# Kernel optimization log

Measured on AMD Instinct MI355X. Metric: run time of the kernel, lower is better.

## Reference

```python
import jax, jax.numpy as jnp
import numpy as np

H = 512
V = 50000
S = 400
B = 64


def setup_inputs() -> dict:
    key = jax.random.key(0)
    ks = jax.random.split(key, 20)
    inp = {
        'input': jax.random.normal(ks[0], (1, B, H), jnp.float32),
        'encoder_states': jax.random.normal(ks[1], (S, B, H), jnp.float32),
        'oov_enc_mask': jax.random.randint(ks[2], (S, B), 0, 2, jnp.int32),
        'hidden': jnp.zeros((1, B, H), jnp.float32),
        # GRU params (PyTorch layout: gates ordered r, z, n)
        'W_ih': jax.random.normal(ks[3], (3 * H, H), jnp.float32) * 0.02,
        'W_hh': jax.random.normal(ks[4], (3 * H, H), jnp.float32) * 0.02,
        'b_ih': jax.random.normal(ks[5], (3 * H,), jnp.float32) * 0.02,
        'b_hh': jax.random.normal(ks[6], (3 * H,), jnp.float32) * 0.02,
        # output vocab projection Linear(2H, V)
        'out_W': jax.random.normal(ks[7], (V, 2 * H), jnp.float32) * 0.02,
        'out_b': jax.random.normal(ks[8], (V,), jnp.float32) * 0.02,
        # additive attention params
        'v': jax.random.normal(ks[9], (H, 1), jnp.float32) * 0.02,
        'Wh': jax.random.normal(ks[10], (H, H), jnp.float32) * 0.02,
        'Ws': jax.random.normal(ks[11], (H, H), jnp.float32) * 0.02,
        'b_attn': jax.random.normal(ks[12], (1, H), jnp.float32) * 0.02,
        # pointer probability Linears (H -> 1)
        'pWh': jax.random.normal(ks[13], (1, H), jnp.float32) * 0.02,
        'pWs': jax.random.normal(ks[14], (1, H), jnp.float32) * 0.02,
        'pWx': jax.random.normal(ks[15], (1, H), jnp.float32) * 0.02,
        'pWx_b': jax.random.normal(ks[16], (1,), jnp.float32) * 0.02,
    }
    return inp


def reference(input, encoder_states, oov_enc_mask, hidden,
              W_ih, W_hh, b_ih, b_hh, out_W, out_b,
              v, Wh, Ws, b_attn, pWh, pWs, pWx, pWx_b):
    x = input[0]            # (B, H)
    h0 = hidden[0]          # (B, H)

    # --- single-step GRU (PyTorch gate order r, z, n) ---
    gi = x @ W_ih.T + b_ih      # (B, 3H)
    gh = h0 @ W_hh.T + b_hh     # (B, 3H)
    ir, iz, inn = jnp.split(gi, 3, axis=1)
    hr, hz, hn = jnp.split(gh, 3, axis=1)
    r = jax.nn.sigmoid(ir + hr)
    z = jax.nn.sigmoid(iz + hz)
    n = jnp.tanh(inn + r * hn)
    h = (1.0 - z) * n + z * h0          # decoder_state, (B, H)
    hidden_new = h[None]                # (1, B, H)

    # --- Bahdanau additive attention, softmax over seq axis ---
    x1 = jnp.einsum('sbh,hk->sbk', encoder_states, Wh)   # (S, B, H)
    x2 = h @ Ws                                          # (B, H) broadcasts over S
    scores = jnp.squeeze(jnp.tanh(x1 + x2 + b_attn) @ v, 2)  # (S, B)
    attn = jax.nn.softmax(scores, axis=0)                # (S, B)
    attn_bs = attn.T                                     # (B, S)

    context = jnp.einsum('bs,sbh->bh', attn_bs, encoder_states)  # (B, H)
    global_state = jnp.concatenate([h, context], axis=1)         # (B, 2H)

    # --- pointer probability ---
    p = jax.nn.sigmoid(context @ pWh.T + h @ pWs.T + x @ pWx.T + pWx_b)  # (B, 1)

    vocab_distr = p * jax.nn.selu(global_state @ out_W.T + out_b)        # (B, V)
    oov_vocab_distr = (1.0 - p) * (attn_bs * oov_enc_mask.astype(jnp.float32).T)  # (B, S)
    extended_vocab_distr = jnp.concatenate([vocab_distr, oov_vocab_distr], axis=1)

    return extended_vocab_distr, hidden_new, jnp.squeeze(p), attn
```

## Files before the change

kernel.cpp:

```cpp
#include <hip/hip_runtime.h>
#include <cmath>

#define H    512
#define H2   1024
#define V    50000
#define SEQ  400
#define EXT  (V + SEQ)

typedef __attribute__((ext_vector_type(8))) short short8;
typedef __attribute__((ext_vector_type(4))) float floatx4;

__device__ __forceinline__ unsigned int bfpack2(float lo, float hi) {
    unsigned int a = __float_as_uint(lo) + 0x8000u;
    unsigned int b = __float_as_uint(hi) + 0x8000u;
    return __builtin_amdgcn_perm(b, a, 0x07060302);
}
__device__ __forceinline__ uint4 pack8(float4 a, float4 b) {
    uint4 r;
    r.x = bfpack2(a.x, a.y);
    r.y = bfpack2(a.z, a.w);
    r.z = bfpack2(b.x, b.y);
    r.w = bfpack2(b.z, b.w);
    return r;
}
__device__ __forceinline__ float4 ld4(const float* p) { return *(const float4*)p; }

__global__ __launch_bounds__(256) void k0_transpose(
    const float* __restrict__ Wh, const float* __restrict__ Ws,
    unsigned short* __restrict__ WhT, unsigned short* __restrict__ WsT)
{
    __shared__ float T[64][65];
    const float* src = blockIdx.z ? Ws : Wh;
    unsigned short* dst = blockIdx.z ? WsT : WhT;
    const int k0 = blockIdx.x * 64, n0 = blockIdx.y * 64;
    const int tid = threadIdx.x;
    #pragma unroll
    for (int i = 0; i < 16; ++i) {
        int e = i * 256 + tid;
        int r = e >> 6, c = e & 63;
        T[r][c] = src[(size_t)(k0 + r) * H + n0 + c];
    }
    __syncthreads();
    #pragma unroll
    for (int i = 0; i < 16; ++i) {
        int e = i * 256 + tid;
        int nn = e >> 6, kk = e & 63;
        unsigned int u = __float_as_uint(T[kk][nn]) + 0x8000u;
        dst[(size_t)(n0 + nn) * H + k0 + kk] = (unsigned short)(u >> 16);
    }
}

__global__ __launch_bounds__(256) void k1_gru_part(
    const float* __restrict__ x, const float* __restrict__ h0,
    const float* __restrict__ W_ih, const float* __restrict__ W_hh,
    float* __restrict__ gacc)
{
    __shared__ uint4 Ax[512];
    __shared__ uint4 Ah[512];
    __shared__ uint4 Bg[6][512];
    const int tid  = threadIdx.x;
    const int wave = tid >> 6, lane = tid & 63;
    const int lrow = lane & 15, q = lane >> 4;
    const int J0   = blockIdx.x * 64;
    const int ks   = blockIdx.y;
    const int kc   = ks * 64;

    #pragma unroll
    for (int c = 0; c < 2; ++c) {
        int idx = c * 256 + tid;
        int m = idx >> 3, j2 = idx & 7, k8 = j2 ^ (m & 7);
        const float* sx = x  + m * H + kc + k8 * 8;
        const float* sh = h0 + m * H + kc + k8 * 8;
        Ax[idx] = pack8(ld4(sx), ld4(sx + 4));
        Ah[idx] = pack8(ld4(sh), ld4(sh + 4));
    }
    #pragma unroll
    for (int g = 0; g < 6; ++g) {
        const float* Wb = (g < 3) ? W_ih : W_hh;
        const int go = (g % 3) * H;
        #pragma unroll
        for (int c = 0; c < 2; ++c) {
            int idx = c * 256 + tid;
            int n = idx >> 3, j2 = idx & 7, k8 = j2 ^ (n & 7);
            const float* sw = Wb + (size_t)(go + J0 + n) * H + kc + k8 * 8;
            Bg[g][idx] = pack8(ld4(sw), ld4(sw + 4));
        }
    }
    __syncthreads();

    floatx4 acc[6];
    #pragma unroll
    for (int g = 0; g < 6; ++g) acc[g] = (floatx4){0.f, 0.f, 0.f, 0.f};
    floatx4 accm[6][4];
    #pragma unroll
    for (int g = 0; g < 6; ++g)
        #pragma unroll
        for (int mt = 0; mt < 4; ++mt) accm[g][mt] = (floatx4){0.f, 0.f, 0.f, 0.f};

    #pragma unroll
    for (int kk8 = 0; kk8 < 8; kk8 += 4) {
        const int k8 = kk8 + q;
        short8 ax[4], ah[4];
        #pragma unroll
        for (int mt = 0; mt < 4; ++mt) {
            int m = mt * 16 + lrow;
            ax[mt] = *(const short8*)&Ax[m * 8 + (k8 ^ (m & 7))];
            ah[mt] = *(const short8*)&Ah[m * 8 + (k8 ^ (m & 7))];
        }
        const int n = wave * 16 + lrow;
        const int gidx = n * 8 + (k8 ^ (n & 7));
        #pragma unroll
        for (int g = 0; g < 6; ++g) {
            short8 bb = *(const short8*)&Bg[g][gidx];
            #pragma unroll
            for (int mt = 0; mt < 4; ++mt)
                accm[g][mt] = __builtin_amdgcn_mfma_f32_16x16x32_bf16(
                    (g < 3) ? ax[mt] : ah[mt], bb, accm[g][mt], 0, 0, 0);
        }
    }
    const int j = J0 + wave * 16 + lrow;
    #pragma unroll
    for (int g = 0; g < 6; ++g)
        #pragma unroll
        for (int mt = 0; mt < 4; ++mt)
            #pragma unroll
            for (int r = 0; r < 4; ++r) {
                const int bb = mt * 16 + q * 4 + r;
                gacc[(((size_t)g * 8 + ks) * 64 + bb) * H + j] = accm[g][mt][r];
            }
}

__global__ __launch_bounds__(256) void k1_gru_fin(
    const float* __restrict__ gacc, const float* __restrict__ h0,
    const float* __restrict__ b_ih, const float* __restrict__ b_hh,
    float* __restrict__ h_out)
{
    const int e = blockIdx.x * 256 + threadIdx.x;
    const int j = e & (H - 1);
    const int b = e >> 9;
    float gs[6];
    #pragma unroll
    for (int g = 0; g < 6; ++g) {
        float sum = 0.f;
        #pragma unroll
        for (int ks = 0; ks < 8; ++ks)
            sum += gacc[(((size_t)g * 8 + ks) * 64 + b) * H + j];
        gs[g] = sum;
    }
    float rg = 1.f / (1.f + expf(-(gs[0] + b_ih[j] + gs[3] + b_hh[j])));
    float zg = 1.f / (1.f + expf(-(gs[1] + b_ih[H + j] + gs[4] + b_hh[H + j])));
    float ng = tanhf(gs[2] + b_ih[2 * H + j] + rg * (gs[5] + b_hh[2 * H + j]));
    float h0v = h0[b * H + j];
    h_out[b * H + j] = (1.f - zg) * ng + zg * h0v;
}

__global__ __launch_bounds__(256) void k2_x2(
    const float* __restrict__ h, const unsigned short* __restrict__ WsT,
    const float* __restrict__ b_attn, float* __restrict__ x2)
{
    __shared__ uint4 Ag[512];
    __shared__ uint4 Bgg[512];
    const int tid  = threadIdx.x;
    const int wave = tid >> 6, lane = tid & 63;
    const int lrow = lane & 15, q = lane >> 4;
    const int n0   = blockIdx.x * 64;

    floatx4 acc[4];
    #pragma unroll
    for (int mt = 0; mt < 4; ++mt) acc[mt] = (floatx4){0.f, 0.f, 0.f, 0.f};

    for (int kc = 0; kc < H; kc += 64) {
        __syncthreads();
        #pragma unroll
        for (int c = 0; c < 2; ++c) {
            int idx = c * 256 + tid;
            int m = idx >> 3, j2 = idx & 7, k8 = j2 ^ (m & 7);
            const float* sh = h + m * H + kc + k8 * 8;
            Ag[idx] = pack8(ld4(sh), ld4(sh + 4));
            Bgg[idx] = *(const uint4*)(WsT + (size_t)(n0 + m) * H + kc + k8 * 8);
        }
        __syncthreads();
        #pragma unroll
        for (int kk8 = 0; kk8 < 8; kk8 += 4) {
            const int k8 = kk8 + q;
            const int n = wave * 16 + lrow;
            short8 bb = *(const short8*)&Bgg[n * 8 + (k8 ^ (n & 7))];
            #pragma unroll
            for (int mt = 0; mt < 4; ++mt) {
                int m = mt * 16 + lrow;
                short8 a = *(const short8*)&Ag[m * 8 + (k8 ^ (m & 7))];
                acc[mt] = __builtin_amdgcn_mfma_f32_16x16x32_bf16(a, bb, acc[mt], 0, 0, 0);
            }
        }
    }
    const int n = n0 + wave * 16 + lrow;
    const float ba = b_attn[n];
    #pragma unroll
    for (int mt = 0; mt < 4; ++mt)
        #pragma unroll
        for (int r = 0; r < 4; ++r) {
            const int bb = mt * 16 + q * 4 + r;
            x2[bb * H + n] = acc[mt][r] + ba;
        }
}

__global__ __launch_bounds__(256) void k3_scores(
    const float* __restrict__ enc, const unsigned short* __restrict__ WhT,
    const float* __restrict__ x2, const float* __restrict__ v,
    float* __restrict__ part)
{
    __shared__ uint4 AsG[512];
    __shared__ uint4 BsG[1024];
    __shared__ float red[256];
    const int s   = blockIdx.x;
    const int nc  = blockIdx.y;
    const int n0  = nc * 128;
    const int tid  = threadIdx.x;
    const int wave = tid >> 6, lane = tid & 63;
    const int lrow = lane & 15, q = lane >> 4;

    floatx4 acc[4][2];
    #pragma unroll
    for (int mt = 0; mt < 4; ++mt)
        #pragma unroll
        for (int nt = 0; nt < 2; ++nt) acc[mt][nt] = (floatx4){0.f, 0.f, 0.f, 0.f};

    const float* Abase = enc + (size_t)s * 64 * H;
    for (int kc = 0; kc < H; kc += 64) {
        __syncthreads();
        #pragma unroll
        for (int c = 0; c < 2; ++c) {
            int idx = c * 256 + tid;
            int m = idx >> 3, k8 = (idx & 7) ^ (m & 7);
            const float* sa = Abase + m * H + kc + k8 * 8;
            AsG[idx] = pack8(ld4(sa), ld4(sa + 4));
        }
        #pragma unroll
        for (int c = 0; c < 4; ++c) {
            int idx = c * 256 + tid;
            int n = idx >> 3, k8 = (idx & 7) ^ (n & 7);
            BsG[idx] = *(const uint4*)(WhT + (size_t)(n0 + n) * H + kc + k8 * 8);
        }
        __syncthreads();
        #pragma unroll
        for (int kk8 = 0; kk8 < 8; kk8 += 4) {
            const int k8 = kk8 + q;
            short8 a[4], b[2];
            #pragma unroll
            for (int mt = 0; mt < 4; ++mt) {
                int m = mt * 16 + lrow;
                a[mt] = *(const short8*)&AsG[m * 8 + (k8 ^ (m & 7))];
            }
            #pragma unroll
            for (int nt = 0; nt < 2; ++nt) {
                int n = wave * 32 + nt * 16 + lrow;
                b[nt] = *(const short8*)&BsG[n * 8 + (k8 ^ (n & 7))];
            }
            #pragma unroll
            for (int mt = 0; mt < 4; ++mt)
                #pragma unroll
                for (int nt = 0; nt < 2; ++nt)
                    acc[mt][nt] = __builtin_amdgcn_mfma_f32_16x16x32_bf16(
                        a[mt], b[nt], acc[mt][nt], 0, 0, 0);
        }
    }
    float val[4][4];
    #pragma unroll
    for (int mt = 0; mt < 4; ++mt) {
        #pragma unroll
        for (int r = 0; r < 4; ++r) {
            const int bb = mt * 16 + q * 4 + r;
            float sum = 0.f;
            #pragma unroll
            for (int nt = 0; nt < 2; ++nt) {
                const int n = n0 + wave * 32 + nt * 16 + lrow;
                sum += tanhf(acc[mt][nt][r] + x2[bb * H + n]) * v[n];
            }
            #pragma unroll
            for (int off = 8; off > 0; off >>= 1) sum += __shfl_down(sum, off, 16);
            val[mt][r] = sum;
        }
    }
    __syncthreads();
    if (lrow == 0) {
        #pragma unroll
        for (int mt = 0; mt < 4; ++mt)
            #pragma unroll
            for (int r = 0; r < 4; ++r)
                red[wave * 64 + mt * 16 + q * 4 + r] = val[mt][r];
    }
    __syncthreads();
    if (tid < 64) {
        float sc = red[tid] + red[64 + tid] + red[128 + tid] + red[192 + tid];
        part[((size_t)nc * SEQ + s) * 64 + tid] = sc;
    }
}

__global__ __launch_bounds__(512) void k4_softmax(
    const float* __restrict__ part, float* __restrict__ attn_out)
{
    const int b = blockIdx.x;
    const int t = threadIdx.x;
    __shared__ float red[8];
    __shared__ float smax, ssum;
    float myv = 0.f, val = -1e30f;
    if (t < SEQ) {
        myv = part[((size_t)0 * SEQ + t) * 64 + b]
            + part[((size_t)1 * SEQ + t) * 64 + b]
            + part[((size_t)2 * SEQ + t) * 64 + b]
            + part[((size_t)3 * SEQ + t) * 64 + b];
        val = myv;
    }
    float m = val;
    #pragma unroll
    for (int off = 32; off > 0; off >>= 1) m = fmaxf(m, __shfl_down(m, off, 64));
    if ((t & 63) == 0) red[t >> 6] = m;
    __syncthreads();
    if (t == 0) {
        float mm = red[0];
        #pragma unroll
        for (int w = 1; w < 8; ++w) mm = fmaxf(mm, red[w]);
        smax = mm;
    }
    __syncthreads();
    float e = (t < SEQ) ? expf(myv - smax) : 0.f;
    float ssv = e;
    #pragma unroll
    for (int off = 32; off > 0; off >>= 1) ssv += __shfl_down(ssv, off, 64);
    if ((t & 63) == 0) red[t >> 6] = ssv;
    __syncthreads();
    if (t == 0) {
        float ss = 0.f;
        #pragma unroll
        for (int w = 0; w < 8; ++w) ss += red[w];
        ssum = ss;
    }
    __syncthreads();
    if (t < SEQ) attn_out[t * 64 + b] = e / ssum;
}

__global__ __launch_bounds__(128) void k5_context(
    const float* __restrict__ enc, const float* __restrict__ attn,
    float* __restrict__ ctxp)
{
    const int b  = blockIdx.x;
    const int hc = blockIdx.y;
    const int sg = blockIdx.z;
    const int t  = threadIdx.x;
    __shared__ float a_s[100];
    if (t < 100) a_s[t] = attn[(sg * 100 + t) * 64 + b];
    __syncthreads();
    const int hh = hc * 128 + t;
    const float* p = enc + ((size_t)(sg * 100) * 64 + b) * H + hh;
    float a0 = 0.f, a1 = 0.f;
    #pragma unroll 5
    for (int i = 0; i < 100; i += 2) {
        a0 += a_s[i]     * p[0];
        a1 += a_s[i + 1] * p[(size_t)64 * H];
        p += (size_t)128 * H;
    }
    ctxp[((size_t)sg * 64 + b) * H + hh] = a0 + a1;
}

__global__ __launch_bounds__(512) void k5b_p(
    const float* __restrict__ ctxp, const float* __restrict__ pWh,
    const float* __restrict__ hdec, const float* __restrict__ pWs,
    const float* __restrict__ x, const float* __restrict__ pWx,
    const float* __restrict__ pWx_b,
    float* __restrict__ ctx, float* __restrict__ p_out, float* __restrict__ p_ws)
{
    const int b = blockIdx.x;
    const int t = threadIdx.x;
    __shared__ float rbuf[8];
    float c = ctxp[((size_t)0 * 64 + b) * H + t]
            + ctxp[((size_t)1 * 64 + b) * H + t]
            + ctxp[((size_t)2 * 64 + b) * H + t]
            + ctxp[((size_t)3 * 64 + b) * H + t];
    ctx[b * H + t] = c;
    float term = c * pWh[t] + hdec[b * H + t] * pWs[t] + x[b * H + t] * pWx[t];
    #pragma unroll
    for (int off = 32; off > 0; off >>= 1) term += __shfl_down(term, off, 64);
    if ((t & 63) == 0) rbuf[t >> 6] = term;
    __syncthreads();
    if (t == 0) {
        float ssv = pWx_b[0];
        #pragma unroll
        for (int w = 0; w < 8; ++w) ssv += rbuf[w];
        float pv = 1.f / (1.f + expf(-ssv));
        p_out[b] = pv;
        p_ws[b]  = pv;
    }
}

__global__ __launch_bounds__(256) void k6_vocab(
    const float* __restrict__ h, const float* __restrict__ ctx,
    const float* __restrict__ outW, const float* __restrict__ outb,
    const float* __restrict__ p_ws, float* __restrict__ ext)
{
    __shared__ uint4 AsG[512];
    __shared__ uint4 BsG[1024];
    __shared__ float p_l[64];
    const int tid  = threadIdx.x;
    const int wave = tid >> 6, lane = tid & 63;
    const int lrow = lane & 15, q = lane >> 4;
    const int v0   = blockIdx.x * 128;

    if (tid < 64) p_l[tid] = p_ws[tid];

    floatx4 acc[4][2];
    #pragma unroll
    for (int mt = 0; mt < 4; ++mt)
        #pragma unroll
        for (int nt = 0; nt < 2; ++nt) acc[mt][nt] = (floatx4){0.f, 0.f, 0.f, 0.f};

    for (int kc = 0; kc < H2; kc += 64) {
        __syncthreads();
        const float* Ab = (kc < H) ? (h + kc) : (ctx + (kc - H));
        #pragma unroll
        for (int c = 0; c < 2; ++c) {
            int idx = c * 256 + tid;
            int m = idx >> 3, k8 = (idx & 7) ^ (m & 7);
            const float* sa = Ab + m * H + k8 * 8;
            AsG[idx] = pack8(ld4(sa), ld4(sa + 4));
        }
        #pragma unroll
        for (int c = 0; c < 4; ++c) {
            int idx = c * 256 + tid;
            int n = idx >> 3, k8 = (idx & 7) ^ (n & 7);
            int vr = v0 + n; if (vr >= V) vr = V - 1;
            const float* sb = outW + (size_t)vr * H2 + kc + k8 * 8;
            BsG[idx] = pack8(ld4(sb), ld4(sb + 4));
        }
        __syncthreads();
        #pragma unroll
        for (int kk8 = 0; kk8 < 8; kk8 += 4) {
            const int k8 = kk8 + q;
            short8 a[4], b[2];
            #pragma unroll
            for (int mt = 0; mt < 4; ++mt) {
                int m = mt * 16 + lrow;
                a[mt] = *(const short8*)&AsG[m * 8 + (k8 ^ (m & 7))];
            }
            #pragma unroll
            for (int nt = 0; nt < 2; ++nt) {
                int n = wave * 32 + nt * 16 + lrow;
                b[nt] = *(const short8*)&BsG[n * 8 + (k8 ^ (n & 7))];
            }
            #pragma unroll
            for (int mt = 0; mt < 4; ++mt)
                #pragma unroll
                for (int nt = 0; nt < 2; ++nt)
                    acc[mt][nt] = __builtin_amdgcn_mfma_f32_16x16x32_bf16(
                        a[mt], b[nt], acc[mt][nt], 0, 0, 0);
        }
    }
    #pragma unroll
    for (int nt = 0; nt < 2; ++nt) {
        const int n = v0 + wave * 32 + nt * 16 + lrow;
        if (n < V) {
            const float ob = outb[n];
            #pragma unroll
            for (int mt = 0; mt < 4; ++mt) {
                #pragma unroll
                for (int r = 0; r < 4; ++r) {
                    const int bb = mt * 16 + q * 4 + r;
                    float zz = acc[mt][nt][r] + ob;
                    float sv = (zz > 0.f) ? 1.0507009873554805f * zz
                                          : 1.7580993408473766f * (expf(zz) - 1.f);
                    ext[(size_t)bb * EXT + n] = p_l[bb] * sv;
                }
            }
        }
    }
}

__global__ __launch_bounds__(256) void k7_oov(
    const float* __restrict__ attn, const int* __restrict__ mask,
    const float* __restrict__ p_ws, float* __restrict__ ext)
{
    int e = blockIdx.x * 256 + threadIdx.x;
    if (e < SEQ * 64) {
        int s = e >> 6, b = e & 63;
        float val = (1.f - p_ws[b]) * attn[e] * (mask[e] ? 1.f : 0.f);
        ext[(size_t)b * EXT + V + s] = val;
    }
}

extern "C" void kernel_launch(void* const* d_in, const int* in_sizes, int n_in,
                              void* d_out, int out_size, void* d_ws, size_t ws_size,
                              hipStream_t stream)
{
    (void)in_sizes; (void)n_in; (void)out_size; (void)ws_size;
    const float* x      = (const float*)d_in[0];
    const float* enc    = (const float*)d_in[1];
    const int*   mask   = (const int*)  d_in[2];
    const float* h0     = (const float*)d_in[3];
    const float* W_ih   = (const float*)d_in[4];
    const float* W_hh   = (const float*)d_in[5];
    const float* b_ih   = (const float*)d_in[6];
    const float* b_hh   = (const float*)d_in[7];
    const float* outW   = (const float*)d_in[8];
    const float* outb   = (const float*)d_in[9];
    const float* v      = (const float*)d_in[10];
    const float* Wh     = (const float*)d_in[11];
    const float* Ws     = (const float*)d_in[12];
    const float* b_attn = (const float*)d_in[13];
    const float* pWh    = (const float*)d_in[14];
    const float* pWs    = (const float*)d_in[15];
    const float* pWx    = (const float*)d_in[16];
    const float* pWx_b  = (const float*)d_in[17];

    float* out        = (float*)d_out;
    float* out_ext    = out;
    float* out_hidden = out + (size_t)64 * EXT;
    float* out_p      = out_hidden + 64 * H;
    float* out_attn   = out_p + 64;

    float* ws       = (float*)d_ws;
    float* ws_x2    = ws;
    float* ws_part  = ws_x2 + 64 * H;
    float* ws_ctxp  = ws_part + 4 * SEQ * 64;
    float* ws_ctx   = ws_ctxp + 4 * 64 * H;
    float* ws_p     = ws_ctx + 64 * H;
    float* ws_gacc  = ws_p + 64;
    unsigned short* ws_whT = (unsigned short*)(ws_gacc + 6 * 8 * 64 * H);
    unsigned short* ws_wsT = ws_whT + (size_t)H * H;

    k0_transpose<<<dim3(8, 8, 2), 256, 0, stream>>>(Wh, Ws, ws_whT, ws_wsT);
    k1_gru_part<<<dim3(8, 8), 256, 0, stream>>>(x, h0, W_ih, W_hh, ws_gacc);
    k1_gru_fin<<<128, 256, 0, stream>>>(ws_gacc, h0, b_ih, b_hh, out_hidden);
    k2_x2<<<8, 256, 0, stream>>>(out_hidden, ws_wsT, b_attn, ws_x2);
    k3_scores<<<dim3(SEQ, 4), 256, 0, stream>>>(enc, ws_whT, ws_x2, v, ws_part);
    k4_softmax<<<64, 512, 0, stream>>>(ws_part, out_attn);
    k5_context<<<dim3(64, 4, 4), 128, 0, stream>>>(enc, out_attn, ws_ctxp);
    k5b_p<<<64, 512, 0, stream>>>(ws_ctxp, pWh, out_hidden, pWs, x, pWx, pWx_b,
                                  ws_ctx, out_p, ws_p);
    k6_vocab<<<(V + 127) / 128, 256, 0, stream>>>(out_hidden, ws_ctx, outW, outb,
                                                  ws_p, out_ext);
    k7_oov<<<(SEQ * 64 + 255) / 256, 256, 0, stream>>>(out_attn, mask, ws_p, out_ext);
}
```

Measured before the change: 472.8 us.

## Fuse small launches, pre-pack bf16 global state, retile scores and vocab GEMMs

Merges the weight transpose into the GRU partial kernel and the OOV scatter into the vocab kernel, cutting two launches. k5b now writes the concatenated [h, context] state as bf16, so the vocab kernel loads it directly instead of converting fp32 on every block. The scores kernel uses 256-column tiles, halving the number of N-chunks and the softmax partial reads. The vocab kernel uses 64-column tiles, giving 782 blocks for better CU fill at the cost of reloading the A tile more often.

```diff
diff --git a/kernel.cpp b/kernel.cpp
--- a/kernel.cpp
+++ b/kernel.cpp
@@ -6,6 +6,7 @@
 #define V    50000
 #define SEQ  400
 #define EXT  (V + SEQ)
+#define NB_V 782
 
 typedef __attribute__((ext_vector_type(8))) short short8;
 typedef __attribute__((ext_vector_type(4))) float floatx4;
@@ -25,45 +26,48 @@
 }
 __device__ __forceinline__ float4 ld4(const float* p) { return *(const float4*)p; }
 
-__global__ __launch_bounds__(256) void k0_transpose(
+__global__ __launch_bounds__(256) void k01_fused(
+    const float* __restrict__ x, const float* __restrict__ h0,
+    const float* __restrict__ W_ih, const float* __restrict__ W_hh,
+    float* __restrict__ gacc,
     const float* __restrict__ Wh, const float* __restrict__ Ws,
     unsigned short* __restrict__ WhT, unsigned short* __restrict__ WsT)
 {
-    __shared__ float T[64][65];
-    const float* src = blockIdx.z ? Ws : Wh;
-    unsigned short* dst = blockIdx.z ? WsT : WhT;
-    const int k0 = blockIdx.x * 64, n0 = blockIdx.y * 64;
+    __shared__ __align__(16) unsigned char smem[65536];
     const int tid = threadIdx.x;
-    #pragma unroll
-    for (int i = 0; i < 16; ++i) {
-        int e = i * 256 + tid;
-        int r = e >> 6, c = e & 63;
-        T[r][c] = src[(size_t)(k0 + r) * H + n0 + c];
-    }
-    __syncthreads();
-    #pragma unroll
-    for (int i = 0; i < 16; ++i) {
-        int e = i * 256 + tid;
-        int nn = e >> 6, kk = e & 63;
-        unsigned int u = __float_as_uint(T[kk][nn]) + 0x8000u;
-        dst[(size_t)(n0 + nn) * H + k0 + kk] = (unsigned short)(u >> 16);
-    }
-}
-
-__global__ __launch_bounds__(256) void k1_gru_part(
-    const float* __restrict__ x, const float* __restrict__ h0,
-    const float* __restrict__ W_ih, const float* __restrict__ W_hh,
-    float* __restrict__ gacc)
-{
-    __shared__ uint4 Ax[512];
-    __shared__ uint4 Ah[512];
-    __shared__ uint4 Bg[6][512];
-    const int tid  = threadIdx.x;
+
+    if (blockIdx.x >= 64) {
+        float (*T)[65] = (float (*)[65])smem;
+        const int e   = blockIdx.x - 64;
+        const int zz  = e >> 6, rem = e & 63;
+        const int k0  = (rem & 7) * 64, n0 = (rem >> 3) * 64;
+        const float* src = zz ? Ws : Wh;
+        unsigned short* dst = zz ? WsT : WhT;
+        #pragma unroll
+        for (int i = 0; i < 16; ++i) {
+            int ee = i * 256 + tid;
+            int r = ee >> 6, c = ee & 63;
+            T[r][c] = src[(size_t)(k0 + r) * H + n0 + c];
+        }
+        __syncthreads();
+        #pragma unroll
+        for (int i = 0; i < 16; ++i) {
+            int ee = i * 256 + tid;
+            int nn = ee >> 6, kk = ee & 63;
+            unsigned int u = __float_as_uint(T[kk][nn]) + 0x8000u;
+            dst[(size_t)(n0 + nn) * H + k0 + kk] = (unsigned short)(u >> 16);
+        }
+        return;
+    }
+
+    uint4* Ax = (uint4*)smem;
+    uint4* Ah = (uint4*)(smem + 8192);
+    uint4 (*Bg)[512] = (uint4 (*)[512])(smem + 16384);
     const int wave = tid >> 6, lane = tid & 63;
     const int lrow = lane & 15, q = lane >> 4;
-    const int J0   = blockIdx.x * 64;
-    const int ks   = blockIdx.y;
-    const int kc   = ks * 64;
+    const int jb = blockIdx.x & 7, ks = blockIdx.x >> 3;
+    const int J0 = jb * 64;
+    const int kc = ks * 64;
 
     #pragma unroll
     for (int c = 0; c < 2; ++c) {
@@ -88,9 +92,6 @@
     }
     __syncthreads();
 
-    floatx4 acc[6];
-    #pragma unroll
-    for (int g = 0; g < 6; ++g) acc[g] = (floatx4){0.f, 0.f, 0.f, 0.f};
     floatx4 accm[6][4];
     #pragma unroll
     for (int g = 0; g < 6; ++g)
@@ -210,20 +211,20 @@
     float* __restrict__ part)
 {
     __shared__ uint4 AsG[512];
-    __shared__ uint4 BsG[1024];
+    __shared__ uint4 BsG[2048];
     __shared__ float red[256];
     const int s   = blockIdx.x;
     const int nc  = blockIdx.y;
-    const int n0  = nc * 128;
+    const int n0  = nc * 256;
     const int tid  = threadIdx.x;
     const int wave = tid >> 6, lane = tid & 63;
     const int lrow = lane & 15, q = lane >> 4;
 
-    floatx4 acc[4][2];
+    floatx4 acc[4][4];
     #pragma unroll
     for (int mt = 0; mt < 4; ++mt)
         #pragma unroll
-        for (int nt = 0; nt < 2; ++nt) acc[mt][nt] = (floatx4){0.f, 0.f, 0.f, 0.f};
+        for (int nt = 0; nt < 4; ++nt) acc[mt][nt] = (floatx4){0.f, 0.f, 0.f, 0.f};
 
     const float* Abase = enc + (size_t)s * 64 * H;
     for (int kc = 0; kc < H; kc += 64) {
@@ -236,7 +237,7 @@
             AsG[idx] = pack8(ld4(sa), ld4(sa + 4));
         }
         #pragma unroll
-        for (int c = 0; c < 4; ++c) {
+        for (int c = 0; c < 8; ++c) {
             int idx = c * 256 + tid;
             int n = idx >> 3, k8 = (idx & 7) ^ (n & 7);
             BsG[idx] = *(const uint4*)(WhT + (size_t)(n0 + n) * H + kc + k8 * 8);
@@ -245,21 +246,21 @@
         #pragma unroll
         for (int kk8 = 0; kk8 < 8; kk8 += 4) {
             const int k8 = kk8 + q;
-            short8 a[4], b[2];
+            short8 a[4], b[4];
             #pragma unroll
             for (int mt = 0; mt < 4; ++mt) {
                 int m = mt * 16 + lrow;
                 a[mt] = *(const short8*)&AsG[m * 8 + (k8 ^ (m & 7))];
             }
             #pragma unroll
-            for (int nt = 0; nt < 2; ++nt) {
-                int n = wave * 32 + nt * 16 + lrow;
+            for (int nt = 0; nt < 4; ++nt) {
+                int n = wave * 64 + nt * 16 + lrow;
                 b[nt] = *(const short8*)&BsG[n * 8 + (k8 ^ (n & 7))];
             }
             #pragma unroll
             for (int mt = 0; mt < 4; ++mt)
                 #pragma unroll
-                for (int nt = 0; nt < 2; ++nt)
+                for (int nt = 0; nt < 4; ++nt)
                     acc[mt][nt] = __builtin_amdgcn_mfma_f32_16x16x32_bf16(
                         a[mt], b[nt], acc[mt][nt], 0, 0, 0);
         }
@@ -272,8 +273,8 @@
             const int bb = mt * 16 + q * 4 + r;
             float sum = 0.f;
             #pragma unroll
-            for (int nt = 0; nt < 2; ++nt) {
-                const int n = n0 + wave * 32 + nt * 16 + lrow;
+            for (int nt = 0; nt < 4; ++nt) {
+                const int n = n0 + wave * 64 + nt * 16 + lrow;
                 sum += tanhf(acc[mt][nt][r] + x2[bb * H + n]) * v[n];
             }
             #pragma unroll
@@ -305,10 +306,8 @@
     __shared__ float smax, ssum;
     float myv = 0.f, val = -1e30f;
     if (t < SEQ) {
-        myv = part[((size_t)0 * SEQ + t) * 64 + b]
-            + part[((size_t)1 * SEQ + t) * 64 + b]
-            + part[((size_t)2 * SEQ + t) * 64 + b]
-            + part[((size_t)3 * SEQ + t) * 64 + b];
+        myv = part[(size_t)t * 64 + b]
+            + part[((size_t)SEQ + t) * 64 + b];
         val = myv;
     }
     float m = val;
@@ -367,7 +366,8 @@
     const float* __restrict__ hdec, const float* __restrict__ pWs,
     const float* __restrict__ x, const float* __restrict__ pWx,
     const float* __restrict__ pWx_b,
-    float* __restrict__ ctx, float* __restrict__ p_out, float* __restrict__ p_ws)
+    float* __restrict__ p_out, float* __restrict__ p_ws,
+    unsigned short* __restrict__ gsb)
 {
     const int b = blockIdx.x;
     const int t = threadIdx.x;
@@ -376,8 +376,10 @@
             + ctxp[((size_t)1 * 64 + b) * H + t]
             + ctxp[((size_t)2 * 64 + b) * H + t]
             + ctxp[((size_t)3 * 64 + b) * H + t];
-    ctx[b * H + t] = c;
-    float term = c * pWh[t] + hdec[b * H + t] * pWs[t] + x[b * H + t] * pWx[t];
+    float hv = hdec[b * H + t];
+    gsb[(size_t)b * H2 + t]     = (unsigned short)((__float_as_uint(hv) + 0x8000u) >> 16);
+    gsb[(size_t)b * H2 + H + t] = (unsigned short)((__float_as_uint(c)  + 0x8000u) >> 16);
+    float term = c * pWh[t] + hv * pWs[t] + x[b * H + t] * pWx[t];
     #pragma unroll
     for (int off = 32; off > 0; off >>= 1) term += __shfl_down(term, off, 64);
     if ((t & 63) == 0) rbuf[t >> 6] = term;
@@ -393,38 +395,42 @@
 }
 
 __global__ __launch_bounds__(256) void k6_vocab(
-    const float* __restrict__ h, const float* __restrict__ ctx,
-    const float* __restrict__ outW, const float* __restrict__ outb,
-    const float* __restrict__ p_ws, float* __restrict__ ext)
-{
+    const unsigned short* __restrict__ gsb, const float* __restrict__ outW,
+    const float* __restrict__ outb, const float* __restrict__ p_ws,
+    const float* __restrict__ attn, const int* __restrict__ mask,
+    float* __restrict__ ext)
+{
+    const int tid = threadIdx.x;
+    if (blockIdx.x >= NB_V) {
+        int e = (blockIdx.x - NB_V) * 256 + tid;
+        int s = e >> 6, b = e & 63;
+        float val = (1.f - p_ws[b]) * attn[e] * (mask[e] ? 1.f : 0.f);
+        ext[(size_t)b * EXT + V + s] = val;
+        return;
+    }
     __shared__ uint4 AsG[512];
-    __shared__ uint4 BsG[1024];
+    __shared__ uint4 BsG[512];
     __shared__ float p_l[64];
-    const int tid  = threadIdx.x;
     const int wave = tid >> 6, lane = tid & 63;
     const int lrow = lane & 15, q = lane >> 4;
-    const int v0   = blockIdx.x * 128;
+    const int v0   = blockIdx.x * 64;
 
     if (tid < 64) p_l[tid] = p_ws[tid];
 
-    floatx4 acc[4][2];
-    #pragma unroll
-    for (int mt = 0; mt < 4; ++mt)
-        #pragma unroll
-        for (int nt = 0; nt < 2; ++nt) acc[mt][nt] = (floatx4){0.f, 0.f, 0.f, 0.f};
+    floatx4 acc[4];
+    #pragma unroll
+    for (int mt = 0; mt < 4; ++mt) acc[mt] = (floatx4){0.f, 0.f, 0.f, 0.f};
 
     for (int kc = 0; kc < H2; kc += 64) {
         __syncthreads();
-        const float* Ab = (kc < H) ? (h + kc) : (ctx + (kc - H));
         #pragma unroll
         for (int c = 0; c < 2; ++c) {
             int idx = c * 256 + tid;
             int m = idx >> 3, k8 = (idx & 7) ^ (m & 7);
-            const float* sa = Ab + m * H + k8 * 8;
-            AsG[idx] = pack8(ld4(sa), ld4(sa + 4));
-        }
-        #pragma unroll
-        for (int c = 0; c < 4; ++c) {
+            AsG[idx] = *(const uint4*)(gsb + (size_t)m * H2 + kc + k8 * 8);
+        }
+        #pragma unroll
+        for (int c = 0; c < 2; ++c) {
             int idx = c * 256 + tid;
             int n = idx >> 3, k8 = (idx & 7) ^ (n & 7);
             int vr = v0 + n; if (vr >= V) vr = V - 1;
@@ -435,54 +441,30 @@
         #pragma unroll
         for (int kk8 = 0; kk8 < 8; kk8 += 4) {
             const int k8 = kk8 + q;
-            short8 a[4], b[2];
+            const int n = wave * 16 + lrow;
+            short8 bb = *(const short8*)&BsG[n * 8 + (k8 ^ (n & 7))];
             #pragma unroll
             for (int mt = 0; mt < 4; ++mt) {
                 int m = mt * 16 + lrow;
-                a[mt] = *(const short8*)&AsG[m * 8 + (k8 ^ (m & 7))];
-            }
-            #pragma unroll
-            for (int nt = 0; nt < 2; ++nt) {
-                int n = wave * 32 + nt * 16 + lrow;
-                b[nt] = *(const short8*)&BsG[n * 8 + (k8 ^ (n & 7))];
-            }
-            #pragma unroll
-            for (int mt = 0; mt < 4; ++mt)
-                #pragma unroll
-                for (int nt = 0; nt < 2; ++nt)
-                    acc[mt][nt] = __builtin_amdgcn_mfma_f32_16x16x32_bf16(
-                        a[mt], b[nt], acc[mt][nt], 0, 0, 0);
-        }
-    }
-    #pragma unroll
-    for (int nt = 0; nt < 2; ++nt) {
-        const int n = v0 + wave * 32 + nt * 16 + lrow;
-        if (n < V) {
-            const float ob = outb[n];
-            #pragma unroll
-            for (int mt = 0; mt < 4; ++mt) {
-                #pragma unroll
-                for (int r = 0; r < 4; ++r) {
-                    const int bb = mt * 16 + q * 4 + r;
-                    float zz = acc[mt][nt][r] + ob;
-                    float sv = (zz > 0.f) ? 1.0507009873554805f * zz
-                                          : 1.7580993408473766f * (expf(zz) - 1.f);
-                    ext[(size_t)bb * EXT + n] = p_l[bb] * sv;
-                }
-            }
-        }
-    }
-}
-
-__global__ __launch_bounds__(256) void k7_oov(
-    const float* __restrict__ attn, const int* __restrict__ mask,
-    const float* __restrict__ p_ws, float* __restrict__ ext)
-{
-    int e = blockIdx.x * 256 + threadIdx.x;
-    if (e < SEQ * 64) {
-        int s = e >> 6, b = e & 63;
-        float val = (1.f - p_ws[b]) * attn[e] * (mask[e] ? 1.f : 0.f);
-        ext[(size_t)b * EXT + V + s] = val;
+                short8 a = *(const short8*)&AsG[m * 8 + (k8 ^ (m & 7))];
+                acc[mt] = __builtin_amdgcn_mfma_f32_16x16x32_bf16(a, bb, acc[mt], 0, 0, 0);
+            }
+        }
+    }
+    const int n = v0 + wave * 16 + lrow;
+    if (n < V) {
+        const float ob = outb[n];
+        #pragma unroll
+        for (int mt = 0; mt < 4; ++mt) {
+            #pragma unroll
+            for (int r = 0; r < 4; ++r) {
+                const int bb = mt * 16 + q * 4 + r;
+                float zz = acc[mt][r] + ob;
+                float sv = (zz > 0.f) ? 1.0507009873554805f * zz
+                                      : 1.7580993408473766f * (expf(zz) - 1.f);
+                ext[(size_t)bb * EXT + n] = p_l[bb] * sv;
+            }
+        }
     }
 }
 
@@ -525,17 +507,17 @@
     float* ws_gacc  = ws_p + 64;
     unsigned short* ws_whT = (unsigned short*)(ws_gacc + 6 * 8 * 64 * H);
     unsigned short* ws_wsT = ws_whT + (size_t)H * H;
-
-    k0_transpose<<<dim3(8, 8, 2), 256, 0, stream>>>(Wh, Ws, ws_whT, ws_wsT);
-    k1_gru_part<<<dim3(8, 8), 256, 0, stream>>>(x, h0, W_ih, W_hh, ws_gacc);
+    unsigned short* ws_gsb = ws_wsT + (size_t)H * H;
+
+    k01_fused<<<192, 256, 0, stream>>>(x, h0, W_ih, W_hh, ws_gacc,
+                                       Wh, Ws, ws_whT, ws_wsT);
     k1_gru_fin<<<128, 256, 0, stream>>>(ws_gacc, h0, b_ih, b_hh, out_hidden);
     k2_x2<<<8, 256, 0, stream>>>(out_hidden, ws_wsT, b_attn, ws_x2);
-    k3_scores<<<dim3(SEQ, 4), 256, 0, stream>>>(enc, ws_whT, ws_x2, v, ws_part);
+    k3_scores<<<dim3(SEQ, 2), 256, 0, stream>>>(enc, ws_whT, ws_x2, v, ws_part);
     k4_softmax<<<64, 512, 0, stream>>>(ws_part, out_attn);
     k5_context<<<dim3(64, 4, 4), 128, 0, stream>>>(enc, out_attn, ws_ctxp);
     k5b_p<<<64, 512, 0, stream>>>(ws_ctxp, pWh, out_hidden, pWs, x, pWx, pWx_b,
-                                  ws_ctx, out_p, ws_p);
-    k6_vocab<<<(V + 127) / 128, 256, 0, stream>>>(out_hidden, ws_ctx, outW, outb,
-                                                  ws_p, out_ext);
-    k7_oov<<<(SEQ * 64 + 255) / 256, 256, 0, stream>>>(out_attn, mask, ws_p, out_ext);
-}
+                                  out_p, ws_p, ws_gsb);
+    k6_vocab<<<NB_V + 100, 256, 0, stream>>>(ws_gsb, outW, outb, ws_p,
+                                             out_attn, mask, out_ext);
+}
```

After: 463.2 us. 1.02x faster.
